# Optimization experiments

Measured on AMD Instinct MI355X. Metric: run time of the kernel, lower is better.

Reference implementation:

```python
import jax, jax.numpy as jnp
import numpy as np
from jax import lax

KH = KW = 3
K = KH * KW
STRIDE = 1
PAD = 1
DIL = 1
GN_GROUPS = 32
EPS = 1e-5


def setup_inputs() -> dict:
    key = jax.random.key(0)
    k0, k1, k2 = jax.random.split(key, 3)
    B, C, H, W = 8, 256, 64, 64
    O = 256
    x = jax.random.normal(k0, (B, C, H, W), jnp.float32)
    # offset-predicting conv (DeformConv2dPack.conv_offset); small weights keep offsets ~O(1)
    w_off = jax.random.normal(k1, (2 * K, C, KH, KW), jnp.float32) * 0.01
    b_off = jnp.zeros((2 * K,), jnp.float32)
    w_dcn = jax.random.normal(k2, (O, C, KH, KW), jnp.float32) * (1.0 / np.sqrt(C * K))
    gamma = jnp.ones((O,), jnp.float32)
    beta = jnp.zeros((O,), jnp.float32)
    return {"x": x, "w_off": w_off, "b_off": b_off, "w_dcn": w_dcn, "gamma": gamma, "beta": beta}


def _deform_conv(x, w_off, b_off, w_dcn):
    B, C, H, W = x.shape
    O = w_dcn.shape[0]
    # offsets via standard conv: [B, 2K, Ho, Wo]; channel layout (k, (dy, dx))
    offset = lax.conv_general_dilated(
        x, w_off, (STRIDE, STRIDE), [(PAD, PAD), (PAD, PAD)],
        rhs_dilation=(DIL, DIL), dimension_numbers=("NCHW", "OIHW", "NCHW"))
    offset = offset + b_off[None, :, None, None]
    Ho, Wo = offset.shape[2], offset.shape[3]
    off = offset.reshape(B, K, 2, Ho, Wo)
    ky = jnp.repeat(jnp.arange(KH), KW)  # [K]
    kx = jnp.tile(jnp.arange(KW), KH)    # [K]
    base_y = (jnp.arange(Ho) * STRIDE - PAD)[None, :, None] + (ky * DIL)[:, None, None]  # [K,Ho,1]
    base_x = (jnp.arange(Wo) * STRIDE - PAD)[None, None, :] + (kx * DIL)[:, None, None]  # [K,1,Wo]
    py = off[:, :, 0] + base_y[None].astype(off.dtype)  # [B,K,Ho,Wo]
    px = off[:, :, 1] + base_x[None].astype(off.dtype)

    def sample_one(xi, py_i, px_i):  # xi [C,H,W]; py/px [K,Ho,Wo]
        y0 = jnp.floor(py_i)
        x0 = jnp.floor(px_i)
        dy = py_i - y0
        dx = px_i - x0
        y0i = y0.astype(jnp.int32)
        x0i = x0.astype(jnp.int32)

        def gather(yi, xj, w):
            valid = (yi >= 0) & (yi < H) & (xj >= 0) & (xj < W)
            yc = jnp.clip(yi, 0, H - 1)
            xc = jnp.clip(xj, 0, W - 1)
            return xi[:, yc, xc] * (w * valid)[None]  # [C,K,Ho,Wo]

        return (gather(y0i, x0i, (1 - dy) * (1 - dx))
                + gather(y0i, x0i + 1, (1 - dy) * dx)
                + gather(y0i + 1, x0i, dy * (1 - dx))
                + gather(y0i + 1, x0i + 1, dy * dx))

    cols = jax.vmap(sample_one)(x, py, px)  # [B,C,K,Ho,Wo]
    y = jnp.einsum("ock,bckp->bop", w_dcn.reshape(O, C, K),
                   cols.reshape(B, C, K, Ho * Wo))
    return y.reshape(B, O, Ho, Wo)


def _group_norm(y, gamma, beta):
    B, O, Ho, Wo = y.shape
    g = y.reshape(B, GN_GROUPS, O // GN_GROUPS, Ho, Wo)
    mean = g.mean(axis=(2, 3, 4), keepdims=True)
    var = g.var(axis=(2, 3, 4), keepdims=True)
    yn = ((g - mean) * lax.rsqrt(var + EPS)).reshape(B, O, Ho, Wo)
    return yn * gamma[None, :, None, None] + beta[None, :, None, None]


def reference(x, w_off, b_off, w_dcn, gamma, beta):
    y = _deform_conv(x, w_off, b_off, w_dcn)
    y = _group_norm(y, gamma, beta)
    return y * jnp.tanh(jax.nn.softplus(y))  # Mish
```

## Files before the change

### kernel.cpp

```cpp
#include <hip/hip_runtime.h>
#include <hip/hip_bf16.h>
#include <math.h>

typedef __bf16 bf16x8 __attribute__((ext_vector_type(8)));
typedef float f32x4 __attribute__((ext_vector_type(4)));
typedef unsigned int u32;
typedef u32 u32x4 __attribute__((ext_vector_type(4)));
typedef u32 u32x2 __attribute__((ext_vector_type(2)));


#define FENCE() __builtin_amdgcn_sched_barrier(0)
#define VMCNT(n) do { asm volatile("s_waitcnt vmcnt(" #n ")" ::: "memory"); FENCE(); } while (0)
#define LGKM0() do { asm volatile("s_waitcnt lgkmcnt(0)" ::: "memory"); FENCE(); } while (0)

__device__ inline u32 pack2bf16(float a, float b) {
  u32 ua = __float_as_uint(a);
  u32 ub = __float_as_uint(b);
  ua += 0x7fffu + ((ua >> 16) & 1u);
  ub += 0x7fffu + ((ub >> 16) & 1u);
  return (ua >> 16) | (ub & 0xffff0000u);
}

__global__ void prep(const float* __restrict__ w_dcn, const float* __restrict__ w_off,
                     unsigned short* __restrict__ wT4, unsigned short* __restrict__ wOffT,
                     float* __restrict__ stats) {
  size_t id = (size_t)blockIdx.x * 256 + threadIdx.x;
  if (id < 589824) {
    int o  = (int)(id / 2304);
    int ck = (int)(id % 2304);
    int k = ck >> 8, c = ck & 255;
    float v = w_dcn[(size_t)(o * 256 + c) * 9 + k];
    u32 uv = __float_as_uint(v);
    uv += 0x7fffu + ((uv >> 16) & 1u);
    int tile = ck >> 6, kk = ck & 63;
    int lin = o * 128 + kk * 2;
    int swz = lin ^ ((o & 7) << 4);
    *(unsigned short*)((char*)wT4 + (size_t)tile * 32768 + swz) = (unsigned short)(uv >> 16);
  } else if (id < 663552) {
    int r = (int)(id - 589824);
    int tile = r >> 11;
    int rr = r & 2047;
    int o = rr >> 6, kk = rr & 63;
    int k = tile >> 2, cc = tile & 3;
    int c = (cc << 6) + kk;
    float v = (o < 18) ? w_off[(size_t)(o * 256 + c) * 9 + k] : 0.f;
    u32 uv = __float_as_uint(v);
    uv += 0x7fffu + ((uv >> 16) & 1u);
    int swz = (o * 128 + kk * 2) ^ ((o & 7) << 4);
    *(unsigned short*)((char*)wOffT + (size_t)tile * 4096 + swz) = (unsigned short)(uv >> 16);
  } else if (id < 664064) {
    stats[id - 663552] = 0.f;
  }
}

__global__ __launch_bounds__(256) void transpose_x(const float* __restrict__ x,
                                                   unsigned short* __restrict__ xT) {
  __shared__ float tl[64][65];
  int bx = blockIdx.x;
  int b = bx >> 8;
  int y = (bx >> 2) & 63;
  int cb = (bx & 3) << 6;
  int t = threadIdx.x;
  int xi = t & 63, cr = t >> 6;
  size_t base = (((size_t)(b * 256 + cb) * 64 + y) << 6);
#pragma unroll
  for (int rep = 0; rep < 16; ++rep) {
    int cl = rep * 4 + cr;
    tl[cl][xi] = x[base + (size_t)cl * 4096 + xi];
  }
  __syncthreads();
  int xw = t & 63, cpair = t >> 6;
#pragma unroll
  for (int r = 0; r < 2; ++r) {
    int cgl = cpair * 2 + r;
    int cg = (cb >> 3) + cgl;
    u32 pk4[4];
#pragma unroll
    for (int i = 0; i < 4; ++i)
      pk4[i] = pack2bf16(tl[cgl * 8 + 2 * i][xw], tl[cgl * 8 + 2 * i + 1][xw]);
    u32x4 v = {pk4[0], pk4[1], pk4[2], pk4[3]};
    *(u32x4*)((char*)xT + (((size_t)b << 21)) + ((size_t)cg << 16) + ((y << 6) + xw) * 16) = v;
  }
}

__global__ __launch_bounds__(512, 2) void conv_offset_mfma(
    const unsigned short* __restrict__ xT, const unsigned short* __restrict__ wOffT,
    float* __restrict__ offs) {
  __shared__ unsigned short A[2][128][64];
  __shared__ unsigned short Bo[2][2048];
  const int bx = blockIdx.x;
  const int lb = ((bx & 7) << 5) + (bx >> 3);
  const int b = lb >> 5;
  const int rp = lb & 31;
  const int t = threadIdx.x;
  const int lane = t & 63, wid = t >> 6;
  const char* xTbB = (const char*)xT + ((size_t)b << 21);
  const int p = t >> 2;
  const int row = (rp << 1) + (p >> 6);
  const int xx = p & 63;
  const int cpl = (t & 3) << 1;

  f32x4 acc[2];
  {
    f32x4 z = {0.f, 0.f, 0.f, 0.f};
    acc[0] = z; acc[1] = z;
  }

  u32x4 ra = {0u,0u,0u,0u}, rb = {0u,0u,0u,0u};

  auto issue = [&](int tt, int d) {
    int k = tt >> 2, cc = tt & 3;
    int ky = k / 3, kx = k - ky * 3;
    int ys = row - 1 + ky;
    int xs = xx - 1 + kx;
    bool ok = ((unsigned)ys < 64u) && ((unsigned)xs < 64u);
    u32x4 z = {0u,0u,0u,0u};
    ra = z; rb = z;
    if (ok) {
      const char* s0 = xTbB + ((size_t)(cc * 8 + cpl) << 16) + (((ys << 6) + xs) << 4);
      ra = *(const u32x4*)s0;
      rb = *(const u32x4*)(s0 + 65536);
    }
    if (wid < 4)
      __builtin_amdgcn_global_load_lds(
          (const __attribute__((address_space(1))) u32*)((const char*)wOffT + ((size_t)tt << 12) + (wid << 10) + (lane << 4)),
          (__attribute__((address_space(3))) u32*)((char*)&Bo[d][0] + (wid << 10)),
          16, 0, 0);
  };
  auto writeA = [&](int d) {
    char* dst = (char*)&A[d][0][0] + p * 128;
    int b0 = (t & 3) << 5;
    int sw = (p & 7) << 4;
    *(u32x4*)(dst + (b0 ^ sw)) = ra;
    *(u32x4*)(dst + ((b0 + 16) ^ sw)) = rb;
  };

  issue(0, 0);
  writeA(0);
  __syncthreads();

  int cur = 0;
  for (int tt = 0; tt < 36; ++tt) {
    if (tt < 35) issue(tt + 1, cur ^ 1);
#pragma unroll
    for (int s = 0; s < 2; ++s) {
      int r16 = (wid << 4) + (lane & 15);
      int kx = (s << 6) + ((lane >> 4) << 4);
      bf16x8 a = *(const bf16x8*)((const char*)&A[cur][0][0] + r16 * 128 + (kx ^ ((r16 & 7) << 4)));
#pragma unroll
      for (int j = 0; j < 2; ++j) {
        int o = (j << 4) + (lane & 15);
        bf16x8 bv = *(const bf16x8*)((const char*)&Bo[cur][0] + o * 128 + (kx ^ ((o & 7) << 4)));
        acc[j] = __builtin_amdgcn_mfma_f32_16x16x32_bf16(a, bv, acc[j], 0, 0, 0);
      }
    }
    if (tt < 35) writeA(cur ^ 1);
    __syncthreads();
    cur ^= 1;
  }

#pragma unroll
  for (int j = 0; j < 2; ++j) {
    int o = (j << 4) + (lane & 15);
    if (o < 18) {
#pragma unroll
      for (int r = 0; r < 4; ++r) {
        int pl = (wid << 4) + ((lane >> 4) << 2) + r;
        offs[((size_t)b * 4096 + (rp << 7) + pl) * 18 + o] = acc[j][r];
      }
    }
  }
}

union ArenaM {
  struct {
    unsigned short A[2][128][64];
    unsigned short Bt[3][16384];
  } m;
  unsigned short ytile[256][136];
};

__global__ __launch_bounds__(512) void dcn_main(
    const unsigned short* __restrict__ xT, const float* __restrict__ offs,
    const float* __restrict__ boff, const unsigned short* __restrict__ wT4,
    unsigned short* __restrict__ yb, float* __restrict__ stats) {
  __shared__ ArenaM ar;
  __shared__ u32 pcor[9][128][2];
  __shared__ float pwt[9][128][4];

  const int bx = blockIdx.x;
  const int lb = ((bx & 7) << 5) + (bx >> 3);
  const int b = lb >> 5;
  const int pxbase = (lb & 31) << 7;
  const int t = threadIdx.x;
  const int lane = t & 63, wid = t >> 6;
  const char* xTbB = (const char*)xT + ((size_t)b << 21);
  const int pxs = ((wid & 1) << 6) + lane;
  const int gp = (wid >> 1) << 1;
  const int wr = wid >> 2, wc = wid & 3;
  const int obase = wc << 6;

  for (int idx = t; idx < 1152; idx += 512) {
    int k = idx >> 7, px = idx & 127;
    int pxg = pxbase + px;
    int yy = pxg >> 6, xx = pxg & 63;
    int ky = k / 3, kx = k - ky * 3;
    const float* op = offs + ((size_t)b * 4096 + pxg) * 18 + k * 2;
    float py = op[0] + boff[k * 2] + (float)(yy - 1 + ky);
    float pxf = op[1] + boff[k * 2 + 1] + (float)(xx - 1 + kx);
    float fy = floorf(py), fx = floorf(pxf);
    float dy = py - fy, dx = pxf - fx;
    int y0 = (int)fy, x0 = (int)fx;
    int y1 = y0 + 1, x1 = x0 + 1;
    float vy0 = ((unsigned)y0 < 64u) ? 1.f : 0.f;
    float vy1 = ((unsigned)y1 < 64u) ? 1.f : 0.f;
    float vx0 = ((unsigned)x0 < 64u) ? 1.f : 0.f;
    float vx1 = ((unsigned)x1 < 64u) ? 1.f : 0.f;
    int y0c = min(max(y0, 0), 63), y1c = min(max(y1, 0), 63);
    int x0c = min(max(x0, 0), 63), x1c = min(max(x1, 0), 63);
    pcor[k][px][0] = (u32)((y0c << 6) + x0c) | ((u32)((y0c << 6) + x1c) << 16);
    pcor[k][px][1] = (u32)((y1c << 6) + x0c) | ((u32)((y1c << 6) + x1c) << 16);
    pwt[k][px][0] = (1.f - dy) * (1.f - dx) * vy0 * vx0;
    pwt[k][px][1] = (1.f - dy) * dx * vy0 * vx1;
    pwt[k][px][2] = dy * (1.f - dx) * vy1 * vx0;
    pwt[k][px][3] = dy * dx * vy1 * vx1;
  }

  f32x4 acc[4][4];
#pragma unroll
  for (int i = 0; i < 4; ++i)
#pragma unroll
    for (int j = 0; j < 4; ++j) {
      f32x4 z = {0.f, 0.f, 0.f, 0.f};
      acc[i][j] = z;
    }

  __syncthreads();

  u32x4 rA[8];

  auto issueA = [&](int tt) {
    int k = tt >> 2, cc = tt & 3;
    u32 c01 = pcor[k][pxs][0], c23 = pcor[k][pxs][1];
    const char* p0 = xTbB + ((size_t)((cc << 3) + gp) << 16);
#pragma unroll
    for (int g = 0; g < 2; ++g) {
      const char* bgp = p0 + ((size_t)g << 16);
      rA[g * 4 + 0] = *(const u32x4*)(bgp + ((size_t)(c01 & 0xffffu) << 4));
      rA[g * 4 + 1] = *(const u32x4*)(bgp + ((size_t)(c01 >> 16) << 4));
      rA[g * 4 + 2] = *(const u32x4*)(bgp + ((size_t)(c23 & 0xffffu) << 4));
      rA[g * 4 + 3] = *(const u32x4*)(bgp + ((size_t)(c23 >> 16) << 4));
    }
  };
  auto issueB = [&](int tt, int bufi) {
    const char* src = (const char*)wT4 + ((size_t)tt << 15) + (wid << 12);
    char* dstb = (char*)&ar.m.Bt[bufi][0] + (wid << 12);
#pragma unroll
    for (int i2 = 0; i2 < 4; ++i2) {
      __builtin_amdgcn_global_load_lds(
          (const __attribute__((address_space(1))) u32*)(src + (i2 << 10) + (lane << 4)),
          (__attribute__((address_space(3))) u32*)(dstb + (i2 << 10)),
          16, 0, 0);
    }
  };
  auto blendA = [&](int tt) {
    int k = tt >> 2;
    f32x4 w = *(const f32x4*)&pwt[k][pxs][0];
    char* dst = (char*)&ar.m.A[tt & 1][0][0] + pxs * 128;
    int sw = (pxs & 7) << 4;
#pragma unroll
    for (int g = 0; g < 2; ++g) {
      u32 o4[4];
#pragma unroll
      for (int e = 0; e < 4; ++e) {
        u32 u0 = rA[g * 4 + 0][e], u1 = rA[g * 4 + 1][e];
        u32 u2 = rA[g * 4 + 2][e], u3 = rA[g * 4 + 3][e];
        float lo = w[0] * __uint_as_float(u0 << 16);
        lo = fmaf(w[1], __uint_as_float(u1 << 16), lo);
        lo = fmaf(w[2], __uint_as_float(u2 << 16), lo);
        lo = fmaf(w[3], __uint_as_float(u3 << 16), lo);
        float hi = w[0] * __uint_as_float(u0 & 0xffff0000u);
        hi = fmaf(w[1], __uint_as_float(u1 & 0xffff0000u), hi);
        hi = fmaf(w[2], __uint_as_float(u2 & 0xffff0000u), hi);
        hi = fmaf(w[3], __uint_as_float(u3 & 0xffff0000u), hi);
        asm("v_cvt_pk_bf16_f32 %0, %1, %2" : "=v"(o4[e]) : "v"(lo), "v"(hi));
      }
      u32x4 ov = {o4[0], o4[1], o4[2], o4[3]};
      *(u32x4*)(dst + (((gp + g) << 4) ^ sw)) = ov;
    }
  };

  issueA(0); FENCE();
  issueB(0, 0); FENCE();
  VMCNT(4);
  blendA(0);
  FENCE();
  issueA(1); FENCE();
  issueB(1, 1); FENCE();
  VMCNT(12);
  LGKM0();
  __builtin_amdgcn_s_barrier();

  int bm3 = 0;
  for (int tt = 0; tt < 36; ++tt) {
    {
      const char* Ab = (const char*)&ar.m.A[tt & 1][0][0];
      const char* Bb = (const char*)&ar.m.Bt[bm3][0];
      __builtin_amdgcn_s_setprio(1);
#pragma unroll
      for (int s = 0; s < 2; ++s) {
        int kx = (s << 6) + ((lane >> 4) << 4);
        bf16x8 a[4], bb[4];
#pragma unroll
        for (int i = 0; i < 4; ++i) {
          int r16 = (wr << 6) + (i << 4) + (lane & 15);
          a[i] = *(const bf16x8*)(Ab + r16 * 128 + (kx ^ ((r16 & 7) << 4)));
        }
#pragma unroll
        for (int j = 0; j < 4; ++j) {
          int o = obase + (j << 4) + (lane & 15);
          bb[j] = *(const bf16x8*)(Bb + o * 128 + (kx ^ ((o & 7) << 4)));
        }
#pragma unroll
        for (int i = 0; i < 4; ++i)
#pragma unroll
          for (int j = 0; j < 4; ++j)
            acc[i][j] = __builtin_amdgcn_mfma_f32_16x16x32_bf16(a[i], bb[j], acc[i][j], 0, 0, 0);
      }
      __builtin_amdgcn_s_setprio(0);
    }
    FENCE();
    if (tt < 35) {
      VMCNT(4);
      blendA(tt + 1);
      FENCE();
      if (tt < 34) {
        issueA(tt + 2); FENCE();
        int bn = bm3 + 2; if (bn >= 3) bn -= 3;
        issueB(tt + 2, bn); FENCE();
      }
    }
    if (tt == 34) { VMCNT(0); }
    else { VMCNT(12); }
    LGKM0();
    __builtin_amdgcn_s_barrier();
    FENCE();
    bm3 = (bm3 == 2) ? 0 : bm3 + 1;
  }

#pragma unroll
  for (int j = 0; j < 4; ++j) {
    float s1 = 0.f, s2 = 0.f;
#pragma unroll
    for (int i = 0; i < 4; ++i)
#pragma unroll
      for (int r = 0; r < 4; ++r) {
        float v = acc[i][j][r];
        s1 += v;
        s2 += v * v;
      }
    s1 += __shfl_xor(s1, 1, 64);  s2 += __shfl_xor(s2, 1, 64);
    s1 += __shfl_xor(s1, 2, 64);  s2 += __shfl_xor(s2, 2, 64);
    s1 += __shfl_xor(s1, 4, 64);  s2 += __shfl_xor(s2, 4, 64);
    s1 += __shfl_xor(s1, 16, 64); s2 += __shfl_xor(s2, 16, 64);
    s1 += __shfl_xor(s1, 32, 64); s2 += __shfl_xor(s2, 32, 64);
    if ((lane & 0x37) == 0) {
      int g = (obase + (j << 4) + (lane & 15)) >> 3;
      atomicAdd(&stats[((b << 5) + g) * 2 + 0], s1);
      atomicAdd(&stats[((b << 5) + g) * 2 + 1], s2);
    }
  }

#pragma unroll
  for (int i = 0; i < 4; ++i)
#pragma unroll
    for (int j = 0; j < 4; ++j) {
      int o = obase + (j << 4) + (lane & 15);
      int pxr = (wr << 6) + (i << 4) + ((lane >> 4) << 2);
      u32 wv0, wv1;
      asm("v_cvt_pk_bf16_f32 %0, %1, %2" : "=v"(wv0) : "v"(acc[i][j][0]), "v"(acc[i][j][1]));
      asm("v_cvt_pk_bf16_f32 %0, %1, %2" : "=v"(wv1) : "v"(acc[i][j][2]), "v"(acc[i][j][3]));
      u32x2 wv = {wv0, wv1};
      *(u32x2*)((char*)ar.ytile + o * 272 + pxr * 2) = wv;
    }
  __syncthreads();
  {
    int o = t >> 1, half = t & 1;
    const char* srcb = (const char*)ar.ytile + o * 272 + (half << 7);
    unsigned short* dst = yb + (((size_t)(b * 256 + o)) << 12) + pxbase + (half << 6);
#pragma unroll
    for (int qq = 0; qq < 8; ++qq)
      *(u32x4*)((char*)dst + (qq << 4)) = *(const u32x4*)(srcb + (qq << 4));
  }
}

__global__ __launch_bounds__(256) void gn_mish(const unsigned short* __restrict__ yb,
                                               const float* __restrict__ stats,
                                               const float* __restrict__ gamma,
                                               const float* __restrict__ beta,
                                               float* __restrict__ out) {
  int v = blockIdx.x * 512 + threadIdx.x;
#pragma unroll
  for (int it = 0; it < 2; ++it, v += 256) {
    int o = (v >> 9) & 255;
    int b = v >> 17;
    float s1 = stats[((b << 5) + (o >> 3)) * 2 + 0];
    float s2 = stats[((b << 5) + (o >> 3)) * 2 + 1];
    float mean = s1 * (1.f / 32768.f);
    float var = s2 * (1.f / 32768.f) - mean * mean;
    float rstd = rsqrtf(var + 1e-5f);
    float ga = gamma[o] * rstd, be = beta[o] - mean * gamma[o] * rstd;
    u32x4 u = *(const u32x4*)(yb + ((size_t)v << 3));
    float res[8];
#pragma unroll
    for (int e = 0; e < 4; ++e) {
      float va = __uint_as_float(u[e] << 16);
      float vb = __uint_as_float(u[e] & 0xffff0000u);
      float v0 = fmaf(va, ga, be);
      float v1 = fmaf(vb, ga, be);
      float e0 = expf(fminf(v0, 15.f));
      float e1 = expf(fminf(v1, 15.f));
      float n0 = e0 * (e0 + 2.f);
      float n1 = e1 * (e1 + 2.f);
      float m0 = v0 * (n0 / (n0 + 2.f));
      float m1 = v1 * (n1 / (n1 + 2.f));
      if (v0 > 15.f) m0 = v0;
      if (v1 > 15.f) m1 = v1;
      res[2 * e] = m0;
      res[2 * e + 1] = m1;
    }
    f32x4 o0 = {res[0], res[1], res[2], res[3]};
    f32x4 o1 = {res[4], res[5], res[6], res[7]};
    float* dst = out + ((size_t)v << 3);
    *(f32x4*)dst = o0;
    *((f32x4*)dst + 1) = o1;
  }
}

extern "C" void kernel_launch(void* const* d_in, const int* in_sizes, int n_in,
                              void* d_out, int out_size, void* d_ws, size_t ws_size,
                              hipStream_t stream) {
  const float* x     = (const float*)d_in[0];
  const float* w_off = (const float*)d_in[1];
  const float* b_off = (const float*)d_in[2];
  const float* w_dcn = (const float*)d_in[3];
  const float* gamma = (const float*)d_in[4];
  const float* beta  = (const float*)d_in[5];
  float* out = (float*)d_out;
  char* ws = (char*)d_ws;
  unsigned short* xT   = (unsigned short*)(ws);
  unsigned short* yb   = (unsigned short*)(ws + 16777216);
  float* offs          = (float*)(ws + 33554432);
  unsigned short* wT4  = (unsigned short*)(ws + 35913728);
  unsigned short* wOffT= (unsigned short*)(ws + 37093376);
  float* stats         = (float*)(ws + 37240832);
  prep<<<dim3(2594), dim3(256), 0, stream>>>(w_dcn, w_off, wT4, wOffT, stats);
  transpose_x<<<dim3(2048), dim3(256), 0, stream>>>(x, xT);
  conv_offset_mfma<<<dim3(256), dim3(512), 0, stream>>>(xT, wOffT, offs);
  dcn_main<<<dim3(256), dim3(512), 0, stream>>>(xT, offs, b_off, wT4, yb, stats);
  gn_mish<<<dim3(2048), dim3(256), 0, stream>>>(yb, stats, gamma, beta, out);
}
```

Measured before the change: 131.9 us.

## Restructure offset conv as split-K per-wave MFMA with LDS reduction; packed blend; reorder dcn loop

The offset conv now runs one output row per 256-thread block. Each wave owns a quarter of the input channels, loads A fragments straight from global into registers with no LDS staging, and double-buffers only the weights. Partial sums are then reduced across waves through LDS. This removes the per-step block barriers and LDS A writes of the old kernel, at the cost of a cross-wave reduction and more blocks. In dcn_main, the blend arithmetic is written with 2-wide float vectors so the compiler can use packed FMA. The blend and prefetch of the next tile are moved ahead of the MFMA block, which changes how load latency overlaps with compute.

```diff
diff --git a/kernel.cpp b/kernel.cpp
--- a/kernel.cpp
+++ b/kernel.cpp
@@ -4,6 +4,7 @@
 
 typedef __bf16 bf16x8 __attribute__((ext_vector_type(8)));
 typedef float f32x4 __attribute__((ext_vector_type(4)));
+typedef float f32x2 __attribute__((ext_vector_type(2)));
 typedef unsigned int u32;
 typedef u32 u32x4 __attribute__((ext_vector_type(4)));
 typedef u32 u32x2 __attribute__((ext_vector_type(2)));
@@ -83,90 +84,113 @@
   }
 }
 
-__global__ __launch_bounds__(512, 2) void conv_offset_mfma(
+__global__ __launch_bounds__(256) void conv_offset_mfma(
     const unsigned short* __restrict__ xT, const unsigned short* __restrict__ wOffT,
     float* __restrict__ offs) {
-  __shared__ unsigned short A[2][128][64];
-  __shared__ unsigned short Bo[2][2048];
+  __shared__ union {
+    unsigned short Bo[4][2][2048];
+    float red[4][64][32];
+  } sm;
   const int bx = blockIdx.x;
-  const int lb = ((bx & 7) << 5) + (bx >> 3);
-  const int b = lb >> 5;
-  const int rp = lb & 31;
+  const int lb = ((bx & 7) << 6) + (bx >> 3);
+  const int b = lb >> 6;
+  const int row = lb & 63;
   const int t = threadIdx.x;
-  const int lane = t & 63, wid = t >> 6;
+  const int lane = t & 63, w = t >> 6;
   const char* xTbB = (const char*)xT + ((size_t)b << 21);
-  const int p = t >> 2;
-  const int row = (rp << 1) + (p >> 6);
-  const int xx = p & 63;
-  const int cpl = (t & 3) << 1;
-
-  f32x4 acc[2];
+
+  f32x4 acc[4][2];
+#pragma unroll
+  for (int i = 0; i < 4; ++i)
+#pragma unroll
+    for (int j = 0; j < 2; ++j) {
+      f32x4 z = {0.f, 0.f, 0.f, 0.f};
+      acc[i][j] = z;
+    }
+
+  auto stageB = [&](int k, int d) {
+    const char* src = (const char*)wOffT + ((size_t)((k << 2) + w) << 12);
+    char* dstb = (char*)&sm.Bo[w][d][0];
+#pragma unroll
+    for (int i2 = 0; i2 < 4; ++i2) {
+      __builtin_amdgcn_global_load_lds(
+          (const __attribute__((address_space(1))) u32*)(src + (i2 << 10) + (lane << 4)),
+          (__attribute__((address_space(3))) u32*)(dstb + (i2 << 10)),
+          16, 0, 0);
+    }
+  };
+
+  stageB(0, 0);
+  u32x4 rA[8];
+  const u32x4 zv = {0u, 0u, 0u, 0u};
+
+  for (int k = 0; k < 9; ++k) {
+    int ky = k / 3, kxv = k - ky * 3;
+    int rowp = row - 1 + ky;
+    bool rok = ((unsigned)rowp < 64u);
+    bool ok[4];
+    if (rok) {
+      int pix[4];
+#pragma unroll
+      for (int pg = 0; pg < 4; ++pg) {
+        int xs = (pg << 4) + (lane & 15) + kxv - 1;
+        ok[pg] = ((unsigned)xs < 64u);
+        int xc = min(max(xs, 0), 63);
+        pix[pg] = (rowp << 6) + xc;
+      }
+#pragma unroll
+      for (int s = 0; s < 2; ++s) {
+        const char* base = xTbB + ((size_t)((w << 3) + (s << 2) + (lane >> 4)) << 16);
+#pragma unroll
+        for (int pg = 0; pg < 4; ++pg)
+          rA[s * 4 + pg] = *(const u32x4*)(base + ((size_t)pix[pg] << 4));
+      }
+    }
+    if (k < 8) stageB(k + 1, (k + 1) & 1);
+    VMCNT(4);
+    if (rok) {
+      const char* Bb = (const char*)&sm.Bo[w][k & 1][0];
+#pragma unroll
+      for (int s = 0; s < 2; ++s) {
+        bf16x8 bb[2];
+        int kx = (s << 6) + ((lane >> 4) << 4);
+#pragma unroll
+        for (int j = 0; j < 2; ++j) {
+          int o = (j << 4) + (lane & 15);
+          bb[j] = *(const bf16x8*)(Bb + o * 128 + (kx ^ ((o & 7) << 4)));
+        }
+#pragma unroll
+        for (int pg = 0; pg < 4; ++pg) {
+          u32x4 av = ok[pg] ? rA[s * 4 + pg] : zv;
+          bf16x8 af = __builtin_bit_cast(bf16x8, av);
+#pragma unroll
+          for (int j = 0; j < 2; ++j)
+            acc[pg][j] = __builtin_amdgcn_mfma_f32_16x16x32_bf16(af, bb[j], acc[pg][j], 0, 0, 0);
+        }
+      }
+    }
+  }
+
+#pragma unroll
+  for (int pg = 0; pg < 4; ++pg)
+#pragma unroll
+    for (int j = 0; j < 2; ++j)
+#pragma unroll
+      for (int r = 0; r < 4; ++r) {
+        int px = (pg << 4) + ((lane >> 4) << 2) + r;
+        int o = (j << 4) + (lane & 15);
+        sm.red[w][px][o] = acc[pg][j][r];
+      }
+  __syncthreads();
   {
-    f32x4 z = {0.f, 0.f, 0.f, 0.f};
-    acc[0] = z; acc[1] = z;
-  }
-
-  u32x4 ra = {0u,0u,0u,0u}, rb = {0u,0u,0u,0u};
-
-  auto issue = [&](int tt, int d) {
-    int k = tt >> 2, cc = tt & 3;
-    int ky = k / 3, kx = k - ky * 3;
-    int ys = row - 1 + ky;
-    int xs = xx - 1 + kx;
-    bool ok = ((unsigned)ys < 64u) && ((unsigned)xs < 64u);
-    u32x4 z = {0u,0u,0u,0u};
-    ra = z; rb = z;
-    if (ok) {
-      const char* s0 = xTbB + ((size_t)(cc * 8 + cpl) << 16) + (((ys << 6) + xs) << 4);
-      ra = *(const u32x4*)s0;
-      rb = *(const u32x4*)(s0 + 65536);
-    }
-    if (wid < 4)
-      __builtin_amdgcn_global_load_lds(
-          (const __attribute__((address_space(1))) u32*)((const char*)wOffT + ((size_t)tt << 12) + (wid << 10) + (lane << 4)),
-          (__attribute__((address_space(3))) u32*)((char*)&Bo[d][0] + (wid << 10)),
-          16, 0, 0);
-  };
-  auto writeA = [&](int d) {
-    char* dst = (char*)&A[d][0][0] + p * 128;
-    int b0 = (t & 3) << 5;
-    int sw = (p & 7) << 4;
-    *(u32x4*)(dst + (b0 ^ sw)) = ra;
-    *(u32x4*)(dst + ((b0 + 16) ^ sw)) = rb;
-  };
-
-  issue(0, 0);
-  writeA(0);
-  __syncthreads();
-
-  int cur = 0;
-  for (int tt = 0; tt < 36; ++tt) {
-    if (tt < 35) issue(tt + 1, cur ^ 1);
-#pragma unroll
-    for (int s = 0; s < 2; ++s) {
-      int r16 = (wid << 4) + (lane & 15);
-      int kx = (s << 6) + ((lane >> 4) << 4);
-      bf16x8 a = *(const bf16x8*)((const char*)&A[cur][0][0] + r16 * 128 + (kx ^ ((r16 & 7) << 4)));
-#pragma unroll
-      for (int j = 0; j < 2; ++j) {
-        int o = (j << 4) + (lane & 15);
-        bf16x8 bv = *(const bf16x8*)((const char*)&Bo[cur][0] + o * 128 + (kx ^ ((o & 7) << 4)));
-        acc[j] = __builtin_amdgcn_mfma_f32_16x16x32_bf16(a, bv, acc[j], 0, 0, 0);
-      }
-    }
-    if (tt < 35) writeA(cur ^ 1);
-    __syncthreads();
-    cur ^= 1;
-  }
-
-#pragma unroll
-  for (int j = 0; j < 2; ++j) {
-    int o = (j << 4) + (lane & 15);
-    if (o < 18) {
-#pragma unroll
-      for (int r = 0; r < 4; ++r) {
-        int pl = (wid << 4) + ((lane >> 4) << 2) + r;
-        offs[((size_t)b * 4096 + (rp << 7) + pl) * 18 + o] = acc[j][r];
+    int px = t >> 2, oq = (t & 3) << 3;
+#pragma unroll
+    for (int e = 0; e < 8; ++e) {
+      int o = oq + e;
+      if (o < 18) {
+        float sv = sm.red[0][px][o] + sm.red[1][px][o]
+                 + sm.red[2][px][o] + sm.red[3][px][o];
+        offs[((size_t)b * 4096 + (row << 6) + px) * 18 + o] = sv;
       }
     }
   }
@@ -266,6 +290,8 @@
   auto blendA = [&](int tt) {
     int k = tt >> 2;
     f32x4 w = *(const f32x4*)&pwt[k][pxs][0];
+    f32x2 w0 = {w[0], w[0]}, w1 = {w[1], w[1]};
+    f32x2 w2 = {w[2], w[2]}, w3 = {w[3], w[3]};
     char* dst = (char*)&ar.m.A[tt & 1][0][0] + pxs * 128;
     int sw = (pxs & 7) << 4;
 #pragma unroll
@@ -275,15 +301,15 @@
       for (int e = 0; e < 4; ++e) {
         u32 u0 = rA[g * 4 + 0][e], u1 = rA[g * 4 + 1][e];
         u32 u2 = rA[g * 4 + 2][e], u3 = rA[g * 4 + 3][e];
-        float lo = w[0] * __uint_as_float(u0 << 16);
-        lo = fmaf(w[1], __uint_as_float(u1 << 16), lo);
-        lo = fmaf(w[2], __uint_as_float(u2 << 16), lo);
-        lo = fmaf(w[3], __uint_as_float(u3 << 16), lo);
-        float hi = w[0] * __uint_as_float(u0 & 0xffff0000u);
-        hi = fmaf(w[1], __uint_as_float(u1 & 0xffff0000u), hi);
-        hi = fmaf(w[2], __uint_as_float(u2 & 0xffff0000u), hi);
-        hi = fmaf(w[3], __uint_as_float(u3 & 0xffff0000u), hi);
-        asm("v_cvt_pk_bf16_f32 %0, %1, %2" : "=v"(o4[e]) : "v"(lo), "v"(hi));
+        f32x2 c0 = {__uint_as_float(u0 << 16), __uint_as_float(u0 & 0xffff0000u)};
+        f32x2 c1 = {__uint_as_float(u1 << 16), __uint_as_float(u1 & 0xffff0000u)};
+        f32x2 c2 = {__uint_as_float(u2 << 16), __uint_as_float(u2 & 0xffff0000u)};
+        f32x2 c3 = {__uint_as_float(u3 << 16), __uint_as_float(u3 & 0xffff0000u)};
+        f32x2 v = c0 * w0;
+        v = c1 * w1 + v;
+        v = c2 * w2 + v;
+        v = c3 * w3 + v;
+        asm("v_cvt_pk_bf16_f32 %0, %1, %2" : "=v"(o4[e]) : "v"(v[0]), "v"(v[1]));
       }
       u32x4 ov = {o4[0], o4[1], o4[2], o4[3]};
       *(u32x4*)(dst + (((gp + g) << 4) ^ sw)) = ov;
@@ -300,9 +326,20 @@
   VMCNT(12);
   LGKM0();
   __builtin_amdgcn_s_barrier();
+  FENCE();
 
   int bm3 = 0;
   for (int tt = 0; tt < 36; ++tt) {
+    if (tt < 35) {
+      VMCNT(4);
+      blendA(tt + 1);
+      FENCE();
+    }
+    if (tt < 34) {
+      issueA(tt + 2); FENCE();
+      int bn = bm3 + 2; if (bn >= 3) bn -= 3;
+      issueB(tt + 2, bn); FENCE();
+    }
     {
       const char* Ab = (const char*)&ar.m.A[tt & 1][0][0];
       const char* Bb = (const char*)&ar.m.Bt[bm3][0];
@@ -330,18 +367,8 @@
       __builtin_amdgcn_s_setprio(0);
     }
     FENCE();
-    if (tt < 35) {
-      VMCNT(4);
-      blendA(tt + 1);
-      FENCE();
-      if (tt < 34) {
-        issueA(tt + 2); FENCE();
-        int bn = bm3 + 2; if (bn >= 3) bn -= 3;
-        issueB(tt + 2, bn); FENCE();
-      }
-    }
     if (tt == 34) { VMCNT(0); }
-    else { VMCNT(12); }
+    else if (tt < 34) { VMCNT(12); }
     LGKM0();
     __builtin_amdgcn_s_barrier();
     FENCE();
@@ -456,7 +483,7 @@
   float* stats         = (float*)(ws + 37240832);
   prep<<<dim3(2594), dim3(256), 0, stream>>>(w_dcn, w_off, wT4, wOffT, stats);
   transpose_x<<<dim3(2048), dim3(256), 0, stream>>>(x, xT);
-  conv_offset_mfma<<<dim3(256), dim3(512), 0, stream>>>(xT, wOffT, offs);
+  conv_offset_mfma<<<dim3(512), dim3(256), 0, stream>>>(xT, wOffT, offs);
   dcn_main<<<dim3(256), dim3(512), 0, stream>>>(xT, offs, b_off, wT4, yb, stats);
   gn_mish<<<dim3(2048), dim3(256), 0, stream>>>(yb, stats, gamma, beta, out);
 }
```

After: 125.7 us. 1.05x faster.
